# Kernel optimization log

Hardware: AMD Instinct MI355X
Metric: run time of the kernel (lower is better)

## Reference

```python
import jax, jax.numpy as jnp
import numpy as np

B, S, HID = 1, 4096, 2048
HQ, HKV, D = 16, 8, 128
G = HQ // HKV
WINDOW = 1024
EPS = 1e-6
ROPE_THETA = 1e6


def setup_inputs() -> dict:
    key = jax.random.key(0)
    ks = jax.random.split(key, 6)
    hidden_states = jax.random.normal(ks[0], (B, S, HID), dtype=jnp.float32)
    Wq = jax.random.normal(ks[1], (HQ * D, HID), dtype=jnp.float32) * 0.02
    Wk = jax.random.normal(ks[2], (HKV * D, HID), dtype=jnp.float32) * 0.02
    Wv = jax.random.normal(ks[3], (HKV * D, HID), dtype=jnp.float32) * 0.02
    Wo = jax.random.normal(ks[4], (HID, HQ * D), dtype=jnp.float32) * 0.02
    q_norm_w = jnp.ones((D,), dtype=jnp.float32)
    k_norm_w = jnp.ones((D,), dtype=jnp.float32)
    # standard RoPE tables
    inv_freq = 1.0 / (ROPE_THETA ** (jnp.arange(0, D, 2, dtype=jnp.float32) / D))
    pos = jnp.arange(S, dtype=jnp.float32)
    freqs = pos[:, None] * inv_freq[None, :]            # [S, D/2]
    emb = jnp.concatenate([freqs, freqs], axis=-1)       # [S, D]
    cos = jnp.cos(emb)[None]                             # [1, S, D]
    sin = jnp.sin(emb)[None]
    return {"hidden_states": hidden_states, "cos": cos, "sin": sin,
            "Wq": Wq, "Wk": Wk, "Wv": Wv, "Wo": Wo,
            "q_norm_w": q_norm_w, "k_norm_w": k_norm_w}


def _rms_norm(x, w):
    var = jnp.mean(jnp.square(x), axis=-1, keepdims=True)
    return w * (x * jax.lax.rsqrt(var + EPS))


def _rotate_half(x):
    x1, x2 = jnp.split(x, 2, axis=-1)
    return jnp.concatenate([-x2, x1], axis=-1)


def reference(hidden_states, cos, sin, Wq, Wk, Wv, Wo, q_norm_w, k_norm_w):
    b, s, _ = hidden_states.shape
    # projections -> [B, H, S, D]
    q = (hidden_states @ Wq.T).reshape(b, s, HQ, D)
    k = (hidden_states @ Wk.T).reshape(b, s, HKV, D)
    v = (hidden_states @ Wv.T).reshape(b, s, HKV, D)
    q = _rms_norm(q, q_norm_w).transpose(0, 2, 1, 3)   # [B,HQ,S,D]
    k = _rms_norm(k, k_norm_w).transpose(0, 2, 1, 3)   # [B,HKV,S,D]
    v = v.transpose(0, 2, 1, 3)
    # RoPE (cos/sin broadcast over head dim)
    c = cos[:, None, :, :]
    sn = sin[:, None, :, :]
    q = q * c + _rotate_half(q) * sn
    k = k * c + _rotate_half(k) * sn
    # GQA: group queries per kv head
    qg = q.reshape(b, HKV, G, s, D)
    scaling = D ** -0.5
    scores = jnp.einsum('bhgqd,bhkd->bhgqk', qg, k) * scaling  # [B,HKV,G,S,S]
    # causal + sliding-window additive mask
    i = jnp.arange(s)[:, None]
    j = jnp.arange(s)[None, :]
    allowed = (j <= i) & (j > i - WINDOW)
    scores = jnp.where(allowed[None, None, None], scores, jnp.float32(-1e9))
    attn = jax.nn.softmax(scores, axis=-1)
    out = jnp.einsum('bhgqk,bhkd->bhgqd', attn, v)     # [B,HKV,G,S,D]
    out = out.reshape(b, HQ, s, D).transpose(0, 2, 1, 3).reshape(b, s, HQ * D)
    return out @ Wo.T
```

## Files before the change

kernel.cpp:

```cpp
#include <hip/hip_runtime.h>

typedef __bf16 bf16;
typedef bf16 bf16x8 __attribute__((ext_vector_type(8)));
typedef bf16 bf16x4 __attribute__((ext_vector_type(4)));
typedef float f32x4 __attribute__((ext_vector_type(4)));

#define MFMA16(a, b, c) __builtin_amdgcn_mfma_f32_16x16x32_bf16((a), (b), (c), 0, 0, 0)

__device__ __forceinline__ void gload_lds16(const bf16* g, bf16* l) {
  __builtin_amdgcn_global_load_lds(
      (const __attribute__((address_space(1))) void*)g,
      (__attribute__((address_space(3))) void*)l, 16, 0, 0);
}

template <int N>
__device__ __forceinline__ void lgkm_fence() {
  if constexpr (N == 0) asm volatile("s_waitcnt lgkmcnt(0)" ::: "memory");
  else if constexpr (N == 4) asm volatile("s_waitcnt lgkmcnt(4)" ::: "memory");
  else if constexpr (N == 8) asm volatile("s_waitcnt lgkmcnt(8)" ::: "memory");
  else if constexpr (N == 12) asm volatile("s_waitcnt lgkmcnt(12)" ::: "memory");
  __builtin_amdgcn_sched_barrier(0);
}
__device__ __forceinline__ void bar_fence() {
  __builtin_amdgcn_sched_barrier(0);
  __builtin_amdgcn_s_barrier();
}

__global__ __launch_bounds__(256) void cvt_all(const float* __restrict__ hid,
                                               const float* __restrict__ wq,
                                               const float* __restrict__ wk,
                                               const float* __restrict__ wv,
                                               const float* __restrict__ wo,
                                               bf16* __restrict__ xbf,
                                               bf16* __restrict__ wcat,
                                               bf16* __restrict__ wob) {
  int j = blockIdx.x * 256 + threadIdx.x;
  const float* src;
  bf16* dst;
  if (j < 2097152) { src = hid; dst = xbf; }
  else {
    j -= 2097152;
    if (j < 1048576) { src = wq; dst = wcat; }
    else {
      j -= 1048576;
      if (j < 524288) { src = wk; dst = wcat + 4194304; }
      else {
        j -= 524288;
        if (j < 524288) { src = wv; dst = wcat + 6291456; }
        else { j -= 524288; src = wo; dst = wob; }
      }
    }
  }
  float4 v = ((const float4*)src)[j];
  bf16x4 o;
  o[0] = (bf16)v.x; o[1] = (bf16)v.y; o[2] = (bf16)v.z; o[3] = (bf16)v.w;
  ((bf16x4*)dst)[j] = o;
}

template <int BM, int BN, int MT, int NTT, int NSPLIT, typename OutT>
__global__ __launch_bounds__(512, 2) void gemm_pipe(const bf16* __restrict__ A,
                                                    const bf16* __restrict__ B,
                                                    OutT* __restrict__ C0,
                                                    OutT* __restrict__ C1,
                                                    int M, int N, int K) {
  constexpr int MH = MT / 2, NH = NTT / 2;
  constexpr int ASLOT = BM * 64;
  constexpr int BSLOT = BN * 64;
  constexpr int NLA = BM / 64, NLB = BN / 64;
  __shared__ __align__(16) bf16 SA[2 * ASLOT];
  __shared__ __align__(16) bf16 SB[2 * BSLOT];

  const int tid = threadIdx.x;
  const int w = tid >> 6, lane = tid & 63;
  const int l15 = lane & 15, quad = lane >> 4;
  const int wr = w >> 2, wc = w & 3;

  const int nbx = N / BN;
  const int nwg = (M / BM) * nbx;
  int bx = (int)blockIdx.x;
  int split = 0;
  if constexpr (NSPLIT > 1) { split = bx / nwg; bx -= split * nwg; }
  const int Keff = K / NSPLIT;
  const int NTILES = Keff >> 6;
  OutT* __restrict__ C = (split ? C1 : C0);
  const bf16* __restrict__ Ab = A + (size_t)split * Keff;
  const bf16* __restrict__ Bb = B + (size_t)split * Keff;

  const int wg = (bx & 7) * (nwg >> 3) + (bx >> 3);
  const int bm0 = (wg / nbx) * BM;
  const int bn0 = (wg % nbx) * BN;

  const int r0 = tid >> 3;
  const int sg = (tid & 7) ^ ((tid >> 3) & 7);
  unsigned aoffg[NLA], boffg[NLB];
#pragma unroll
  for (int i = 0; i < NLA; ++i)
    aoffg[i] = (unsigned)((bm0 + r0 + i * 64) * K + sg * 8);
#pragma unroll
  for (int i = 0; i < NLB; ++i)
    boffg[i] = (unsigned)((bn0 + r0 + i * 64) * K + sg * 8);

  const int xl = l15 & 7;
  const int p0 = quad ^ xl;
  const int baseA0 = (wr * (MT * 16) + l15) * 128 + p0 * 16;
  const int baseA1 = (wr * (MT * 16) + l15) * 128 + ((p0 ^ 4) * 16);
  const int baseB0 = (wc * (NTT * 16) + l15) * 128 + p0 * 16;
  const int baseB1 = (wc * (NTT * 16) + l15) * 128 + ((p0 ^ 4) * 16);
  const char* saB = (const char*)&SA[0];
  const char* sbB = (const char*)&SB[0];

  f32x4 acc[MT][NTT] = {};
  bf16x8 As[2][MH][2];
  bf16x8 Bs[2][NH][2];

#define LDA_(SL, H, DST)                                                        \
  _Pragma("unroll") for (int mt = 0; mt < MH; ++mt) {                           \
    (DST)[mt][0] = *(const bf16x8*)(saB + (SL) * (ASLOT * 2) + baseA0 +         \
                                    ((H) * MH + mt) * 2048);                    \
    (DST)[mt][1] = *(const bf16x8*)(saB + (SL) * (ASLOT * 2) + baseA1 +         \
                                    ((H) * MH + mt) * 2048);                    \
  }
#define LDB_(SL, G, DST)                                                        \
  _Pragma("unroll") for (int nt = 0; nt < NH; ++nt) {                           \
    (DST)[nt][0] = *(const bf16x8*)(sbB + (SL) * (BSLOT * 2) + baseB0 +         \
                                    ((G) * NH + nt) * 2048);                    \
    (DST)[nt][1] = *(const bf16x8*)(sbB + (SL) * (BSLOT * 2) + baseB1 +         \
                                    ((G) * NH + nt) * 2048);                    \
  }
#define QMFMA_(AS, BS, MHI, NHI)                                                \
  __builtin_amdgcn_s_setprio(1);                                                \
  _Pragma("unroll") for (int mt = 0; mt < MH; ++mt)                             \
      _Pragma("unroll") for (int nt = 0; nt < NH; ++nt) {                       \
    acc[(MHI) * MH + mt][(NHI) * NH + nt] = MFMA16(                             \
        (AS)[mt][0], (BS)[nt][0], acc[(MHI) * MH + mt][(NHI) * NH + nt]);       \
    acc[(MHI) * MH + mt][(NHI) * NH + nt] = MFMA16(                             \
        (AS)[mt][1], (BS)[nt][1], acc[(MHI) * MH + mt][(NHI) * NH + nt]);       \
  }                                                                             \
  __builtin_amdgcn_s_setprio(0);
#define STAGE_(SO, TS)                                                          \
  _Pragma("unroll") for (int i = 0; i < NLA; ++i)                               \
      gload_lds16(Ab + aoffg[i] + (TS) * 64, SA + (SO) * ASLOT + tid * 8 + i * 4096); \
  _Pragma("unroll") for (int i = 0; i < NLB; ++i)                               \
      gload_lds16(Bb + boffg[i] + (TS) * 64, SB + (SO) * BSLOT + tid * 8 + i * 4096);

#define GTILE_BODY(PAR, TS)                                                     \
  {                                                                             \
    constexpr int sl_ = (PAR), so_ = (PAR) ^ 1;                                 \
    constexpr int e0_ = (PAR), e1_ = (PAR) ^ 1;                                 \
                                                                        \
    LDB_(sl_, 1, Bs[e1_]);                                                      \
    bar_fence();                                                                \
    lgkm_fence<NTT>();                                                          \
    if ((TS) < NTILES) { STAGE_(so_, (TS)); }                                   \
    QMFMA_(As[0], Bs[e0_], 0, 0);                                               \
                                                                        \
    LDA_(sl_, 1, As[1]);                                                        \
    bar_fence();                                                                \
    lgkm_fence<MT>();                                                           \
    QMFMA_(As[0], Bs[e1_], 0, 1);                                               \
                                                                        \
    LDB_(sl_, 0, Bs[e0_]);                                                      \
    asm volatile("s_waitcnt vmcnt(0)" ::: "memory");                            \
    bar_fence();                                                                \
    lgkm_fence<NTT>();                                                          \
    QMFMA_(As[1], Bs[e1_], 1, 1);                                               \
                                                                        \
    LDA_(so_, 0, As[0]);                                                        \
    LDB_(so_, 0, Bs[e1_]);                                                      \
    bar_fence();                                                                \
    lgkm_fence<MT + NTT>();                                                     \
    QMFMA_(As[1], Bs[e0_], 1, 0);                                               \
  }

  { STAGE_(0, 0); }
  asm volatile("s_waitcnt vmcnt(0)" ::: "memory");
  bar_fence();
  __builtin_amdgcn_sched_barrier(0);
  LDA_(0, 0, As[0]);
  LDB_(0, 0, Bs[0]);

  for (int t = 0; t < NTILES; t += 2) {
    GTILE_BODY(0, t + 1);
    GTILE_BODY(1, t + 2);
  }

#undef LDA_
#undef LDB_
#undef QMFMA_
#undef STAGE_
#undef GTILE_BODY

#pragma unroll
  for (int mt = 0; mt < MT; ++mt)
#pragma unroll
    for (int nt = 0; nt < NTT; ++nt) {
      int row = bm0 + wr * (MT * 16) + mt * 16 + quad * 4;
      int col = bn0 + wc * (NTT * 16) + nt * 16 + l15;
#pragma unroll
      for (int r = 0; r < 4; ++r)
        C[(size_t)(row + r) * N + col] = (OutT)acc[mt][nt][r];
    }
}

__global__ __launch_bounds__(256) void addred(const float4* __restrict__ p0,
                                              const float4* __restrict__ p1,
                                              float4* __restrict__ out, int n4) {
  int i = blockIdx.x * 256 + threadIdx.x;
  if (i < n4) {
    float4 a = p0[i], b = p1[i];
    float4 o;
    o.x = a.x + b.x; o.y = a.y + b.y; o.z = a.z + b.z; o.w = a.w + b.w;
    out[i] = o;
  }
}

__global__ __launch_bounds__(256) void prep(const bf16* __restrict__ QKVb,
                                            const float* __restrict__ cosb,
                                            const float* __restrict__ sinb,
                                            const float* __restrict__ qw,
                                            const float* __restrict__ kw,
                                            bf16* __restrict__ Qb,
                                            bf16* __restrict__ Kb,
                                            bf16* __restrict__ Vtp) {
  __shared__ __align__(16) bf16 T[64 * 136];
  const int b = blockIdx.x;
  const int tid = threadIdx.x;
  if (b < 512) {
    const int kvh = b >> 6;
    const int s0 = (b & 63) * 64;
    for (int g = tid; g < 1024; g += 256) {
      int s = g >> 4, cg = g & 15;
      *(bf16x8*)(T + s * 136 + cg * 8) =
          *(const bf16x8*)(QKVb + (size_t)(s0 + s) * 4096 + 3072 + kvh * 128 + cg * 8);
    }
    __syncthreads();
    for (int g = tid; g < 1024; g += 256) {
      int d = g >> 3, sg = g & 7;
      bf16x8 v;
#pragma unroll
      for (int j = 0; j < 8; j++) {
        int kp = sg * 8 + j;
        int s = (kp & 3) * 16 + (kp >> 2);
        v[j] = T[s * 136 + d];
      }
      *(bf16x8*)(Vtp + ((size_t)kvh * 128 + d) * 4096 + s0 + sg * 8) = v;
    }
  } else {
    const int wid = ((b - 512) * 256 + tid) >> 6;
    const int lane = tid & 63;
    const int s = wid / 24;
    const int h = wid % 24;
    const bool isq = (h < 16);
    const int col0 = isq ? h * 128 : 2048 + (h - 16) * 128;
    const float* wt = isq ? qw : kw;

    const bf16* row = QKVb + (size_t)s * 4096 + col0;
    float x1 = (float)row[lane];
    float x2 = (float)row[lane + 64];

    float ss = x1 * x1 + x2 * x2;
#pragma unroll
    for (int m = 32; m >= 1; m >>= 1) ss += __shfl_xor(ss, m, 64);
    float rs = rsqrtf(ss * (1.0f / 128.0f) + 1e-6f);

    float c = cosb[(size_t)s * 128 + lane];
    float sn = sinb[(size_t)s * 128 + lane];
    float xn1 = x1 * rs * wt[lane];
    float xn2 = x2 * rs * wt[lane + 64];
    float o1 = xn1 * c - xn2 * sn;
    float o2 = xn2 * c + xn1 * sn;
    const float scale = isq ? 0.12751652f : 1.0f;
    o1 *= scale; o2 *= scale;

    bf16* dst = isq ? (Qb + ((size_t)h * 4096 + s) * 128)
                    : (Kb + ((size_t)(h - 16) * 4096 + s) * 128);
    dst[lane] = (bf16)o1;
    dst[lane + 64] = (bf16)o2;
  }
}

__global__ __launch_bounds__(512, 1) void attn_kernel(const bf16* __restrict__ Qb,
                                                      const bf16* __restrict__ Kb,
                                                      const bf16* __restrict__ Vtp,
                                                      bf16* __restrict__ Ob) {
  const int SEQ = 4096, W = 1024;
  const float MP = 17.312340f;
  __shared__ __align__(16) bf16 Ks[2][64 * 128];
  __shared__ __align__(16) bf16 Vs[2][128 * 64];
  __shared__ __align__(16) bf16 Ps[8][32 * 64];

  const int id = blockIdx.x;
  const int kvh = id & 7, gq = (id >> 3) & 1, h = kvh * 2 + gq;
  const int qb0 = (id >> 4) * 256;
  const int tid = threadIdx.x, w = tid >> 6, lane = tid & 63;
  const int l15 = lane & 15, quad = lane >> 4;
  const int qw0 = qb0 + w * 32;

  bf16x8 qf[2][4];
#pragma unroll
  for (int m = 0; m < 2; m++) {
    const bf16* qp = Qb + ((size_t)h * SEQ + qw0 + m * 16 + l15) * 128 + quad * 8;
#pragma unroll
    for (int kb = 0; kb < 4; kb++) qf[m][kb] = *(const bf16x8*)(qp + kb * 32);
  }

  f32x4 o[2][8] = {};
  f32x4 lr[2] = {};
  bf16* pw = &Ps[w][0];
  const bf16* kbase = Kb + (size_t)kvh * SEQ * 128;
  const bf16* vbase = Vtp + (size_t)kvh * 128 * SEQ;

  int jmin = qb0 - (W - 1); if (jmin < 0) jmin = 0;
  const int kt0 = jmin >> 6, kt1 = (qb0 + 255) >> 6;

#define ASTAGE(KT, SL)                                                          \
  do {                                                                          \
    const int k0_ = (KT) * 64;                                                  \
    _Pragma("unroll") for (int i_ = 0; i_ < 2; ++i_) {                          \
      int slot = i_ * 512 + tid;                                                \
      int key = slot >> 4, gg = slot & 15;                                      \
      int gsw = gg ^ (key & 7);                                                 \
      gload_lds16(kbase + (size_t)(k0_ + key) * 128 + gsw * 8,                  \
                  &Ks[SL][0] + slot * 8);                                       \
    }                                                                           \
    _Pragma("unroll") for (int i_ = 0; i_ < 2; ++i_) {                          \
      int slot = i_ * 512 + tid;                                                \
      int d = slot >> 3, gg = slot & 7;                                         \
      int gsw = gg ^ (d & 7);                                                   \
      gload_lds16(vbase + (size_t)d * SEQ + k0_ + gsw * 8,                      \
                  &Vs[SL][0] + slot * 8);                                       \
    }                                                                           \
  } while (0)

  ASTAGE(kt0, 0);

  for (int kt = kt0; kt <= kt1; ++kt) {
    const int sl = (kt - kt0) & 1;
    if (kt < kt1) {
      ASTAGE(kt + 1, sl ^ 1);
      asm volatile("s_waitcnt vmcnt(4)" ::: "memory");
    } else {
      asm volatile("s_waitcnt vmcnt(0)" ::: "memory");
    }
    __builtin_amdgcn_s_barrier();

    const int k0 = kt * 64;
    const bf16* ks = &Ks[sl][0];
    const bf16* vs = &Vs[sl][0];
    const bool alive = (k0 <= qw0 + 31) && (k0 + 63 > qw0 - W);
    if (alive) {
      const bool full = (k0 + 63 <= qw0) && (k0 > qw0 + 31 - W);
      f32x4 s[2][4] = {};
#pragma unroll
      for (int c = 0; c < 4; c++) {
        const int key = c * 16 + l15;
        bf16x8 kf[4];
#pragma unroll
        for (int kb = 0; kb < 4; kb++)
          kf[kb] = *(const bf16x8*)(ks + key * 128 + (((kb * 4 + quad) ^ (key & 7)) << 3));
        __builtin_amdgcn_s_setprio(1);
#pragma unroll
        for (int kb = 0; kb < 4; kb++) {
          s[0][c] = MFMA16(qf[0][kb], kf[kb], s[0][c]);
          s[1][c] = MFMA16(qf[1][kb], kf[kb], s[1][c]);
        }
        __builtin_amdgcn_s_setprio(0);
      }
#pragma unroll
      for (int m = 0; m < 2; m++)
#pragma unroll
        for (int r = 0; r < 4; r++) {
          float p[4];
          if (full) {
#pragma unroll
            for (int c = 0; c < 4; c++) p[c] = __builtin_amdgcn_exp2f(s[m][c][r] - MP);
          } else {
            const int i_ = qw0 + m * 16 + quad * 4 + r;
#pragma unroll
            for (int c = 0; c < 4; c++) {
              int j = k0 + c * 16 + l15;
              p[c] = (j <= i_ && j > i_ - W) ? __builtin_amdgcn_exp2f(s[m][c][r] - MP) : 0.0f;
            }
          }
          lr[m][r] += p[0] + p[1] + p[2] + p[3];
          bf16x4 pk;
          pk[0] = (bf16)p[0]; pk[1] = (bf16)p[1]; pk[2] = (bf16)p[2]; pk[3] = (bf16)p[3];
          const int qrow = m * 16 + quad * 4 + r;
          *(bf16x4*)(pw + qrow * 64 + (((l15 >> 1) ^ (qrow & 7)) << 3) + (l15 & 1) * 4) = pk;
        }
      asm volatile("s_waitcnt lgkmcnt(0)" ::: "memory");
      bf16x8 pf[2][2];
#pragma unroll
      for (int m = 0; m < 2; m++)
#pragma unroll
        for (int kb = 0; kb < 2; kb++)
          pf[m][kb] = *(const bf16x8*)(pw + (m * 16 + l15) * 64 +
                                       (((kb * 4 + quad) ^ (l15 & 7)) << 3));
#pragma unroll
      for (int n = 0; n < 8; n++) {
        const int d = n * 16 + l15;
        bf16x8 vf0 = *(const bf16x8*)(vs + d * 64 + ((quad ^ (l15 & 7)) << 3));
        bf16x8 vf1 = *(const bf16x8*)(vs + d * 64 + (((4 + quad) ^ (l15 & 7)) << 3));
        __builtin_amdgcn_s_setprio(1);
        o[0][n] = MFMA16(pf[0][0], vf0, o[0][n]);
        o[0][n] = MFMA16(pf[0][1], vf1, o[0][n]);
        o[1][n] = MFMA16(pf[1][0], vf0, o[1][n]);
        o[1][n] = MFMA16(pf[1][1], vf1, o[1][n]);
        __builtin_amdgcn_s_setprio(0);
      }
    }
    __builtin_amdgcn_s_barrier();
  }
#undef ASTAGE

  float linv[2][4];
#pragma unroll
  for (int m = 0; m < 2; m++)
#pragma unroll
    for (int r = 0; r < 4; r++) {
      float v = lr[m][r];
      v += __shfl_xor(v, 1, 64);
      v += __shfl_xor(v, 2, 64);
      v += __shfl_xor(v, 4, 64);
      v += __shfl_xor(v, 8, 64);
      linv[m][r] = 1.0f / v;
    }
#pragma unroll
  for (int m = 0; m < 2; m++)
#pragma unroll
    for (int n = 0; n < 8; n++)
#pragma unroll
      for (int r = 0; r < 4; r++) {
        int i_ = qw0 + m * 16 + quad * 4 + r;
        Ob[(size_t)i_ * 2048 + h * 128 + n * 16 + l15] = (bf16)(o[m][n][r] * linv[m][r]);
      }
}

extern "C" void kernel_launch(void* const* d_in, const int* in_sizes, int n_in,
                              void* d_out, int out_size, void* d_ws, size_t ws_size,
                              hipStream_t stream) {
  const float* hid  = (const float*)d_in[0];
  const float* cosb = (const float*)d_in[1];
  const float* sinb = (const float*)d_in[2];
  const float* Wq   = (const float*)d_in[3];
  const float* Wk   = (const float*)d_in[4];
  const float* Wv   = (const float*)d_in[5];
  const float* Wo   = (const float*)d_in[6];
  const float* qw   = (const float*)d_in[7];
  const float* kw   = (const float*)d_in[8];

  if (ws_size < (size_t)(112u) * 1024u * 1024u) return;

  char* ws = (char*)d_ws;
  bf16* Xbf  = (bf16*)(ws);
  bf16* Vtp  = (bf16*)(ws);
  float* P1  = (float*)(ws);
  bf16* Wcat = (bf16*)(ws + (16u << 20));
  bf16* Wob  = (bf16*)(ws + (32u << 20));
  bf16* QKVb = (bf16*)(ws + (40u << 20));
  float* P0  = (float*)(ws + (40u << 20));
  bf16* Qb   = (bf16*)(ws + (72u << 20));
  bf16* Kb   = (bf16*)(ws + (88u << 20));
  bf16* Ob   = (bf16*)(ws + (96u << 20));

  cvt_all<<<20480, 256, 0, stream>>>(hid, Wq, Wk, Wv, Wo, Xbf, Wcat, Wob);

  gemm_pipe<256, 256, 8, 4, 1, bf16><<<256, 512, 0, stream>>>(
      Xbf, Wcat, QKVb, QKVb, 4096, 4096, 2048);

  prep<<<25088, 256, 0, stream>>>(QKVb, cosb, sinb, qw, kw, Qb, Kb, Vtp);

  attn_kernel<<<256, 512, 0, stream>>>(Qb, Kb, Vtp, Ob);

  gemm_pipe<256, 256, 8, 4, 2, float><<<256, 512, 0, stream>>>(
      Ob, Wob, P0, P1, 4096, 2048, 2048);
  addred<<<8192, 256, 0, stream>>>((const float4*)P0, (const float4*)P1,
                                   (float4*)d_out, 2097152);
}
```

Measured before the change: 329.8 us.

## Replace pipelined 16x16 MFMA GEMM with simpler 32x32x16 MFMA GEMM

Both projection GEMMs now use a new kernel built on 32x32x16 bf16 MFMA instructions, with each wave computing a 128x64 output tile as 4x2 fragments. The hand-scheduled quarter-tile pipeline with explicit lgkm/vmcnt fences and register double-buffering is dropped in favour of a plain double-buffered LDS loop with __syncthreads. The aim is fewer LDS reads per FLOP and fewer MFMA issues. The cost is losing the fine-grained overlap of LDS reads with MFMA, and the new 32-lane-row epilogue writes columns in a less coalesced pattern.

Result: no change. 334.4 us (+1.4%).

```diff
diff --git a/kernel.cpp b/kernel.cpp
--- a/kernel.cpp
+++ b/kernel.cpp
@@ -4,26 +4,15 @@
 typedef bf16 bf16x8 __attribute__((ext_vector_type(8)));
 typedef bf16 bf16x4 __attribute__((ext_vector_type(4)));
 typedef float f32x4 __attribute__((ext_vector_type(4)));
+typedef float f32x16 __attribute__((ext_vector_type(16)));
 
 #define MFMA16(a, b, c) __builtin_amdgcn_mfma_f32_16x16x32_bf16((a), (b), (c), 0, 0, 0)
+#define MFMA32(a, b, c) __builtin_amdgcn_mfma_f32_32x32x16_bf16((a), (b), (c), 0, 0, 0)
 
 __device__ __forceinline__ void gload_lds16(const bf16* g, bf16* l) {
   __builtin_amdgcn_global_load_lds(
       (const __attribute__((address_space(1))) void*)g,
       (__attribute__((address_space(3))) void*)l, 16, 0, 0);
-}
-
-template <int N>
-__device__ __forceinline__ void lgkm_fence() {
-  if constexpr (N == 0) asm volatile("s_waitcnt lgkmcnt(0)" ::: "memory");
-  else if constexpr (N == 4) asm volatile("s_waitcnt lgkmcnt(4)" ::: "memory");
-  else if constexpr (N == 8) asm volatile("s_waitcnt lgkmcnt(8)" ::: "memory");
-  else if constexpr (N == 12) asm volatile("s_waitcnt lgkmcnt(12)" ::: "memory");
-  __builtin_amdgcn_sched_barrier(0);
-}
-__device__ __forceinline__ void bar_fence() {
-  __builtin_amdgcn_sched_barrier(0);
-  __builtin_amdgcn_s_barrier();
 }
 
 __global__ __launch_bounds__(256) void cvt_all(const float* __restrict__ hid,
@@ -57,148 +46,104 @@
   ((bf16x4*)dst)[j] = o;
 }
 
-template <int BM, int BN, int MT, int NTT, int NSPLIT, typename OutT>
-__global__ __launch_bounds__(512, 2) void gemm_pipe(const bf16* __restrict__ A,
-                                                    const bf16* __restrict__ B,
-                                                    OutT* __restrict__ C0,
-                                                    OutT* __restrict__ C1,
-                                                    int M, int N, int K) {
-  constexpr int MH = MT / 2, NH = NTT / 2;
-  constexpr int ASLOT = BM * 64;
-  constexpr int BSLOT = BN * 64;
-  constexpr int NLA = BM / 64, NLB = BN / 64;
+template <int NSPLIT, typename OutT>
+__global__ __launch_bounds__(512, 2) void gemm32(const bf16* __restrict__ A,
+                                                 const bf16* __restrict__ B,
+                                                 OutT* __restrict__ C0,
+                                                 OutT* __restrict__ C1,
+                                                 int M, int N, int K) {
+  constexpr int ASLOT = 256 * 64;
+  constexpr int BSLOT = 256 * 64;
   __shared__ __align__(16) bf16 SA[2 * ASLOT];
   __shared__ __align__(16) bf16 SB[2 * BSLOT];
 
   const int tid = threadIdx.x;
   const int w = tid >> 6, lane = tid & 63;
-  const int l15 = lane & 15, quad = lane >> 4;
+  const int l31 = lane & 31, lh = lane >> 5;
   const int wr = w >> 2, wc = w & 3;
 
-  const int nbx = N / BN;
-  const int nwg = (M / BM) * nbx;
+  const int nbx = N >> 8;
+  const int nwg = (M >> 8) * nbx;
   int bx = (int)blockIdx.x;
   int split = 0;
   if constexpr (NSPLIT > 1) { split = bx / nwg; bx -= split * nwg; }
   const int Keff = K / NSPLIT;
-  const int NTILES = Keff >> 6;
+  const int NT = Keff >> 6;
   OutT* __restrict__ C = (split ? C1 : C0);
   const bf16* __restrict__ Ab = A + (size_t)split * Keff;
   const bf16* __restrict__ Bb = B + (size_t)split * Keff;
 
   const int wg = (bx & 7) * (nwg >> 3) + (bx >> 3);
-  const int bm0 = (wg / nbx) * BM;
-  const int bn0 = (wg % nbx) * BN;
+  const int bm0 = (wg / nbx) << 8;
+  const int bn0 = (wg % nbx) << 8;
 
   const int r0 = tid >> 3;
-  const int sg = (tid & 7) ^ ((tid >> 3) & 7);
-  unsigned aoffg[NLA], boffg[NLB];
-#pragma unroll
-  for (int i = 0; i < NLA; ++i)
+  const int sg = (tid & 7) ^ (r0 & 7);
+  unsigned aoffg[4], boffg[4];
+#pragma unroll
+  for (int i = 0; i < 4; ++i) {
     aoffg[i] = (unsigned)((bm0 + r0 + i * 64) * K + sg * 8);
-#pragma unroll
-  for (int i = 0; i < NLB; ++i)
     boffg[i] = (unsigned)((bn0 + r0 + i * 64) * K + sg * 8);
-
-  const int xl = l15 & 7;
-  const int p0 = quad ^ xl;
-  const int baseA0 = (wr * (MT * 16) + l15) * 128 + p0 * 16;
-  const int baseA1 = (wr * (MT * 16) + l15) * 128 + ((p0 ^ 4) * 16);
-  const int baseB0 = (wc * (NTT * 16) + l15) * 128 + p0 * 16;
-  const int baseB1 = (wc * (NTT * 16) + l15) * 128 + ((p0 ^ 4) * 16);
-  const char* saB = (const char*)&SA[0];
-  const char* sbB = (const char*)&SB[0];
-
-  f32x4 acc[MT][NTT] = {};
-  bf16x8 As[2][MH][2];
-  bf16x8 Bs[2][NH][2];
-
-#define LDA_(SL, H, DST)                                                        \
-  _Pragma("unroll") for (int mt = 0; mt < MH; ++mt) {                           \
-    (DST)[mt][0] = *(const bf16x8*)(saB + (SL) * (ASLOT * 2) + baseA0 +         \
-                                    ((H) * MH + mt) * 2048);                    \
-    (DST)[mt][1] = *(const bf16x8*)(saB + (SL) * (ASLOT * 2) + baseA1 +         \
-                                    ((H) * MH + mt) * 2048);                    \
-  }
-#define LDB_(SL, G, DST)                                                        \
-  _Pragma("unroll") for (int nt = 0; nt < NH; ++nt) {                           \
-    (DST)[nt][0] = *(const bf16x8*)(sbB + (SL) * (BSLOT * 2) + baseB0 +         \
-                                    ((G) * NH + nt) * 2048);                    \
-    (DST)[nt][1] = *(const bf16x8*)(sbB + (SL) * (BSLOT * 2) + baseB1 +         \
-                                    ((G) * NH + nt) * 2048);                    \
-  }
-#define QMFMA_(AS, BS, MHI, NHI)                                                \
-  __builtin_amdgcn_s_setprio(1);                                                \
-  _Pragma("unroll") for (int mt = 0; mt < MH; ++mt)                             \
-      _Pragma("unroll") for (int nt = 0; nt < NH; ++nt) {                       \
-    acc[(MHI) * MH + mt][(NHI) * NH + nt] = MFMA16(                             \
-        (AS)[mt][0], (BS)[nt][0], acc[(MHI) * MH + mt][(NHI) * NH + nt]);       \
-    acc[(MHI) * MH + mt][(NHI) * NH + nt] = MFMA16(                             \
-        (AS)[mt][1], (BS)[nt][1], acc[(MHI) * MH + mt][(NHI) * NH + nt]);       \
-  }                                                                             \
-  __builtin_amdgcn_s_setprio(0);
-#define STAGE_(SO, TS)                                                          \
-  _Pragma("unroll") for (int i = 0; i < NLA; ++i)                               \
-      gload_lds16(Ab + aoffg[i] + (TS) * 64, SA + (SO) * ASLOT + tid * 8 + i * 4096); \
-  _Pragma("unroll") for (int i = 0; i < NLB; ++i)                               \
-      gload_lds16(Bb + boffg[i] + (TS) * 64, SB + (SO) * BSLOT + tid * 8 + i * 4096);
-
-#define GTILE_BODY(PAR, TS)                                                     \
-  {                                                                             \
-    constexpr int sl_ = (PAR), so_ = (PAR) ^ 1;                                 \
-    constexpr int e0_ = (PAR), e1_ = (PAR) ^ 1;                                 \
-                                                                        \
-    LDB_(sl_, 1, Bs[e1_]);                                                      \
-    bar_fence();                                                                \
-    lgkm_fence<NTT>();                                                          \
-    if ((TS) < NTILES) { STAGE_(so_, (TS)); }                                   \
-    QMFMA_(As[0], Bs[e0_], 0, 0);                                               \
-                                                                        \
-    LDA_(sl_, 1, As[1]);                                                        \
-    bar_fence();                                                                \
-    lgkm_fence<MT>();                                                           \
-    QMFMA_(As[0], Bs[e1_], 0, 1);                                               \
-                                                                        \
-    LDB_(sl_, 0, Bs[e0_]);                                                      \
-    asm volatile("s_waitcnt vmcnt(0)" ::: "memory");                            \
-    bar_fence();                                                                \
-    lgkm_fence<NTT>();                                                          \
-    QMFMA_(As[1], Bs[e1_], 1, 1);                                               \
-                                                                        \
-    LDA_(so_, 0, As[0]);                                                        \
-    LDB_(so_, 0, Bs[e1_]);                                                      \
-    bar_fence();                                                                \
-    lgkm_fence<MT + NTT>();                                                     \
-    QMFMA_(As[1], Bs[e0_], 1, 0);                                               \
-  }
-
-  { STAGE_(0, 0); }
-  asm volatile("s_waitcnt vmcnt(0)" ::: "memory");
-  bar_fence();
-  __builtin_amdgcn_sched_barrier(0);
-  LDA_(0, 0, As[0]);
-  LDB_(0, 0, Bs[0]);
-
-  for (int t = 0; t < NTILES; t += 2) {
-    GTILE_BODY(0, t + 1);
-    GTILE_BODY(1, t + 2);
-  }
-
-#undef LDA_
-#undef LDB_
-#undef QMFMA_
-#undef STAGE_
-#undef GTILE_BODY
-
-#pragma unroll
-  for (int mt = 0; mt < MT; ++mt)
-#pragma unroll
-    for (int nt = 0; nt < NTT; ++nt) {
-      int row = bm0 + wr * (MT * 16) + mt * 16 + quad * 4;
-      int col = bn0 + wc * (NTT * 16) + nt * 16 + l15;
-#pragma unroll
-      for (int r = 0; r < 4; ++r)
-        C[(size_t)(row + r) * N + col] = (OutT)acc[mt][nt][r];
+  }
+
+  int arow[4], brow[2], koff[4];
+#pragma unroll
+  for (int m = 0; m < 4; ++m) arow[m] = (wr * 128 + m * 32 + l31) * 64;
+#pragma unroll
+  for (int n = 0; n < 2; ++n) brow[n] = (wc * 64 + n * 32 + l31) * 64;
+#pragma unroll
+  for (int ks = 0; ks < 4; ++ks) koff[ks] = ((2 * ks + lh) ^ (lane & 7)) << 3;
+
+  f32x16 acc[4][2] = {};
+
+#define STAGE32_(SO, TS)                                                        \
+  _Pragma("unroll") for (int i_ = 0; i_ < 4; ++i_)                              \
+      gload_lds16(Ab + aoffg[i_] + (TS) * 64,                                   \
+                  SA + (SO) * ASLOT + tid * 8 + i_ * 4096);                     \
+  _Pragma("unroll") for (int i_ = 0; i_ < 4; ++i_)                              \
+      gload_lds16(Bb + boffg[i_] + (TS) * 64,                                   \
+                  SB + (SO) * BSLOT + tid * 8 + i_ * 4096)
+
+  STAGE32_(0, 0);
+  __syncthreads();
+
+  for (int t = 0; t < NT; ++t) {
+    const int sl = t & 1;
+    if (t + 1 < NT) { STAGE32_(sl ^ 1, t + 1); }
+    const bf16* sa = SA + sl * ASLOT;
+    const bf16* sb = SB + sl * BSLOT;
+#pragma unroll
+    for (int ks = 0; ks < 4; ++ks) {
+      bf16x8 af[4], bfr[2];
+#pragma unroll
+      for (int m = 0; m < 4; ++m)
+        af[m] = *(const bf16x8*)(sa + arow[m] + koff[ks]);
+#pragma unroll
+      for (int n = 0; n < 2; ++n)
+        bfr[n] = *(const bf16x8*)(sb + brow[n] + koff[ks]);
+      __builtin_amdgcn_s_setprio(1);
+#pragma unroll
+      for (int m = 0; m < 4; ++m)
+#pragma unroll
+        for (int n = 0; n < 2; ++n)
+          acc[m][n] = MFMA32(af[m], bfr[n], acc[m][n]);
+      __builtin_amdgcn_s_setprio(0);
+    }
+    __syncthreads();
+  }
+#undef STAGE32_
+
+#pragma unroll
+  for (int mf = 0; mf < 4; ++mf)
+#pragma unroll
+    for (int nf = 0; nf < 2; ++nf) {
+      const int rb = bm0 + wr * 128 + mf * 32 + 4 * lh;
+      const int cb = bn0 + wc * 64 + nf * 32 + l31;
+#pragma unroll
+      for (int r = 0; r < 16; ++r) {
+        int row = rb + (r & 3) + 8 * (r >> 2);
+        C[(size_t)row * N + cb] = (OutT)acc[mf][nf][r];
+      }
     }
 }
 
@@ -465,15 +410,13 @@
 
   cvt_all<<<20480, 256, 0, stream>>>(hid, Wq, Wk, Wv, Wo, Xbf, Wcat, Wob);
 
-  gemm_pipe<256, 256, 8, 4, 1, bf16><<<256, 512, 0, stream>>>(
-      Xbf, Wcat, QKVb, QKVb, 4096, 4096, 2048);
+  gemm32<1, bf16><<<256, 512, 0, stream>>>(Xbf, Wcat, QKVb, QKVb, 4096, 4096, 2048);
 
   prep<<<25088, 256, 0, stream>>>(QKVb, cosb, sinb, qw, kw, Qb, Kb, Vtp);
 
   attn_kernel<<<256, 512, 0, stream>>>(Qb, Kb, Vtp, Ob);
 
-  gemm_pipe<256, 256, 8, 4, 2, float><<<256, 512, 0, stream>>>(
-      Ob, Wob, P0, P1, 4096, 2048, 2048);
+  gemm32<2, float><<<256, 512, 0, stream>>>(Ob, Wob, P0, P1, 4096, 2048, 2048);
   addred<<<8192, 256, 0, stream>>>((const float4*)P0, (const float4*)P1,
                                    (float4*)d_out, 2097152);
 }
```
